# Performance work log

Hardware: AMD Instinct MI355X
Metric: run time of the kernel (lower is better)

Reference implementation:

```python
import jax, jax.numpy as jnp
import numpy as np

H = 8  # num_heads


def _ln(x, g, b):
    mu = x.mean(-1, keepdims=True)
    var = ((x - mu) ** 2).mean(-1, keepdims=True)
    return (x - mu) * jax.lax.rsqrt(var + 1e-5) * g + b


def setup_inputs() -> dict:
    key = jax.random.key(0)
    ks = jax.random.split(key, 24)
    B, N, V, E, D, R, L = 8, 512, 50000, 300, 256, 100, 4
    dh = D // H
    s = 0.02
    inp = {}
    inp['token_ids'] = jax.random.randint(ks[0], (B, N), 0, V, dtype=jnp.int32)
    inp['relations'] = jax.random.randint(ks[1], (B, N, N), 0, R, dtype=jnp.int32)
    m = jax.random.bernoulli(ks[2], 0.9, (B, N, N))
    eye = jnp.eye(N, dtype=bool)[None]
    inp['relations_mask'] = jnp.logical_or(m, eye)  # keep diagonal valid so every row attends somewhere
    inp['embed'] = jax.random.normal(ks[3], (V, E), jnp.float32) * s
    inp['W_in'] = jax.random.normal(ks[4], (E, D), jnp.float32) * s
    inp['b_in'] = jnp.zeros((D,), jnp.float32)
    inp['Wq'] = jax.random.normal(ks[5], (L, D, D), jnp.float32) * s
    inp['Wk'] = jax.random.normal(ks[6], (L, D, D), jnp.float32) * s
    inp['Wv'] = jax.random.normal(ks[7], (L, D, D), jnp.float32) * s
    inp['Wo'] = jax.random.normal(ks[8], (L, D, D), jnp.float32) * s
    inp['ln1_g'] = jnp.ones((L, D), jnp.float32)
    inp['ln1_b'] = jnp.zeros((L, D), jnp.float32)
    inp['ln2_g'] = jnp.ones((L, D), jnp.float32)
    inp['ln2_b'] = jnp.zeros((L, D), jnp.float32)
    inp['W1'] = jax.random.normal(ks[9], (L, D, 4 * D), jnp.float32) * s
    inp['b1'] = jnp.zeros((L, 4 * D), jnp.float32)
    inp['W2'] = jax.random.normal(ks[10], (L, 4 * D, D), jnp.float32) * s
    inp['b2'] = jnp.zeros((L, D), jnp.float32)
    inp['rel_k_emb'] = jax.random.normal(ks[11], (R, dh), jnp.float32) * s
    inp['rel_v_emb'] = jax.random.normal(ks[12], (R, dh), jnp.float32) * s
    inp['W_out'] = jax.random.normal(ks[13], (D, D), jnp.float32) * s
    inp['b_out'] = jnp.zeros((D,), jnp.float32)
    return inp


def reference(token_ids, relations, relations_mask, embed, W_in, b_in, Wq, Wk, Wv, Wo,
              ln1_g, ln1_b, ln2_g, ln2_b, W1, b1, W2, b2, rel_k_emb, rel_v_emb, W_out, b_out):
    # Input layer: embedding lookup + projection to gnn hidden size.
    x = embed[token_ids]                          # [B,N,E]
    x = jax.nn.relu(x @ W_in + b_in)              # [B,N,D]
    B, N, D = x.shape
    dh = D // H
    # Shared relation embeddings (share_layers=True, share_heads=True): gathered once.
    rk = rel_k_emb[relations]                     # [B,N,N,dh]
    rv = rel_v_emb[relations]                     # [B,N,N,dh]
    neg = jnp.asarray(-1e9, x.dtype)
    scale = jnp.asarray(1.0 / np.sqrt(dh), x.dtype)
    L = Wq.shape[0]
    for l in range(L):  # fixed small layer count
        q = (x @ Wq[l]).reshape(B, N, H, dh).transpose(0, 2, 1, 3)
        k = (x @ Wk[l]).reshape(B, N, H, dh).transpose(0, 2, 1, 3)
        v = (x @ Wv[l]).reshape(B, N, H, dh).transpose(0, 2, 1, 3)
        # Relation-aware scores: q.k + q.r_k (RAT-SQL)
        scores = (jnp.einsum('bhnd,bhmd->bhnm', q, k)
                  + jnp.einsum('bhnd,bnmd->bhnm', q, rk)) * scale
        scores = jnp.where(relations_mask[:, None], scores, neg)
        a = jax.nn.softmax(scores, axis=-1)       # [B,H,N,N]
        z = (jnp.einsum('bhnm,bhmd->bhnd', a, v)
             + jnp.einsum('bhnm,bnmd->bhnd', a, rv))
        z = z.transpose(0, 2, 1, 3).reshape(B, N, D) @ Wo[l]
        x = _ln(x + z, ln1_g[l], ln1_b[l])
        f = jax.nn.relu(x @ W1[l] + b1[l]) @ W2[l] + b2[l]
        x = _ln(x + f, ln2_g[l], ln2_b[l])
    # Output layer projection
    return x @ W_out + b_out
```

## Files before the change

### kernel.cpp

```cpp
#include <hip/hip_runtime.h>
#include <hip/hip_bf16.h>

#define NTOK 4096
#define NN   512

typedef __attribute__((ext_vector_type(8))) short bf16x8;
typedef __attribute__((ext_vector_type(4))) short bf16x4;
typedef __attribute__((ext_vector_type(4))) float f32x4;

__device__ __forceinline__ float bf16_to_f(unsigned short u) {
    unsigned int x = ((unsigned int)u) << 16;
    return __builtin_bit_cast(float, x);
}
__device__ __forceinline__ unsigned short f_to_bf16(float f) {
    unsigned int b = __builtin_bit_cast(unsigned int, f);
    return (unsigned short)((b + 0x7fff + ((b >> 16) & 1)) >> 16);
}
__device__ __forceinline__ bf16x8 pack8(float4 a, float4 b) {
    bf16x8 v;
    v[0]=(short)f_to_bf16(a.x); v[1]=(short)f_to_bf16(a.y);
    v[2]=(short)f_to_bf16(a.z); v[3]=(short)f_to_bf16(a.w);
    v[4]=(short)f_to_bf16(b.x); v[5]=(short)f_to_bf16(b.y);
    v[6]=(short)f_to_bf16(b.z); v[7]=(short)f_to_bf16(b.w);
    return v;
}

__global__ void detect_mask_kernel(const unsigned char* __restrict__ m, int* __restrict__ flag) {
    __shared__ int f;
    if (threadIdx.x == 0) f = 0;
    __syncthreads();
    int any = 0;
    for (int i = threadIdx.x; i < 4096; i += 256) {
        if ((i & 3) != 0 && m[i] != 0) any = 1;
    }
    if (any) atomicOr(&f, 1);
    __syncthreads();
    if (threadIdx.x == 0) *flag = f;
}

__global__ __launch_bounds__(256) void prep_rel16(
    const int* __restrict__ rel, const void* __restrict__ mask,
    const int* __restrict__ flag, short* __restrict__ rel16)
{
    const bool mbyte = (*flag != 0);
    const unsigned char* m8 = (const unsigned char*)mask;
    const int* m32 = (const int*)mask;
    const int i = (blockIdx.x * 256 + threadIdx.x) * 2;
    int2 rv = *(const int2*)(rel + i);
    int ok0, ok1;
    if (mbyte) { ok0 = m8[i]; ok1 = m8[i + 1]; }
    else       { ok0 = (m32[i] != 0); ok1 = (m32[i + 1] != 0); }
    short2 o;
    o.x = ok0 ? (short)rv.x : (short)-1;
    o.y = ok1 ? (short)rv.y : (short)-1;
    *(short2*)(rel16 + i) = o;
}

__global__ __launch_bounds__(256) void embed_proj_kernel(
    const int* __restrict__ tok, const float* __restrict__ embed,
    const float* __restrict__ W_in, const float* __restrict__ b_in,
    float* __restrict__ x)
{
    __shared__ float emb[8][304];
    __shared__ int tloc[8];
    const int t = threadIdx.x;
    const int r0 = blockIdx.x * 8;
    if (t < 8) tloc[t] = tok[r0 + t];
    __syncthreads();
    for (int i = t; i < 8 * 300; i += 256) {
        int r = i / 300, e = i - r * 300;
        emb[r][e] = embed[(size_t)tloc[r] * 300 + e];
    }
    __syncthreads();
    float acc[8] = {0.f,0.f,0.f,0.f,0.f,0.f,0.f,0.f};
    const int d = t;
    for (int e = 0; e < 300; ++e) {
        float w = W_in[e * 256 + d];
#pragma unroll
        for (int r = 0; r < 8; ++r) acc[r] += emb[r][e] * w;
    }
    const float bb = b_in[d];
#pragma unroll
    for (int r = 0; r < 8; ++r) {
        float o = acc[r] + bb;
        o = o > 0.f ? o : 0.f;
        x[(size_t)(r0 + r) * 256 + d] = o;
    }
}

__global__ __launch_bounds__(256) void gemm_mfma(
    const float* __restrict__ A,
    const float* __restrict__ W0, const float* __restrict__ W1p, const float* __restrict__ W2p,
    int ncPerW, const float* __restrict__ bias,
    float* __restrict__ C, int M, int K, int Nc, int relu)
{
    __shared__ unsigned short As[64][40];
    __shared__ unsigned short Bs[64][40];

    const int t = threadIdx.x;
    const int lane = t & 63, w = t >> 6;
    const int g = lane >> 4, li = lane & 15;
    const int r0 = blockIdx.y * 64, c0 = blockIdx.x * 64;

    const float* Wp = W0; int cW = c0;
    if (c0 >= 2 * ncPerW)      { Wp = W2p; cW = c0 - 2 * ncPerW; }
    else if (c0 >= ncPerW)     { Wp = W1p; cW = c0 - ncPerW; }

    f32x4 acc[4];
#pragma unroll
    for (int i = 0; i < 4; ++i) acc[i] = (f32x4){0.f, 0.f, 0.f, 0.f};

    const int arow = t >> 2, ad8 = (t & 3) * 8;
    const int bnn = t & 63, bk8 = (t >> 6) * 8;

    for (int k0 = 0; k0 < K; k0 += 32) {
        __syncthreads();
        {
            const float* ap = A + (size_t)(r0 + arow) * K + k0 + ad8;
            float4 a0 = *(const float4*)ap;
            float4 a1 = *(const float4*)(ap + 4);
            *(bf16x8*)&As[arow][ad8] = pack8(a0, a1);
        }
        {
            bf16x8 v;
#pragma unroll
            for (int j = 0; j < 8; ++j) {
                float xv = Wp[(size_t)(k0 + bk8 + j) * ncPerW + cW + bnn];
                v[j] = (short)f_to_bf16(xv);
            }
            *(bf16x8*)&Bs[bnn][bk8] = v;
        }
        __syncthreads();
        bf16x8 af = *(const bf16x8*)&As[16 * w + li][g * 8];
#pragma unroll
        for (int sub = 0; sub < 4; ++sub) {
            bf16x8 bfr = *(const bf16x8*)&Bs[16 * sub + li][g * 8];
            acc[sub] = __builtin_amdgcn_mfma_f32_16x16x32_bf16(af, bfr, acc[sub], 0, 0, 0);
        }
    }
#pragma unroll
    for (int sub = 0; sub < 4; ++sub) {
        int col = c0 + sub * 16 + li;
        float bv = bias ? bias[col] : 0.f;
#pragma unroll
        for (int r = 0; r < 4; ++r) {
            int row = r0 + 16 * w + g * 4 + r;
            float o = acc[sub][r] + bv;
            if (relu) o = fmaxf(o, 0.f);
            C[(size_t)row * Nc + col] = o;
        }
    }
}

__global__ __launch_bounds__(256) void attn_mfma(
    const float* __restrict__ qkv,
    const short* __restrict__ rel16,
    const float* __restrict__ relk_g,
    const float* __restrict__ relv_g,
    float* __restrict__ zout)
{
    const int b = blockIdx.z, h = blockIdx.y, n0 = blockIdx.x * 64;
    const int t = threadIdx.x;
    const int lane = t & 63, w = t >> 6;
    const int g = lane >> 4, li = lane & 15;

    __shared__ float wrel[64][100];
    __shared__ unsigned short qrk[64][100];
    __shared__ union {
        unsigned short relk_s[100][40];
        unsigned short relvT[32][136];
        struct {
            unsigned short k_t[32][40];
            unsigned short v_t[32][40];
            short rel_t[64][36];
            unsigned short p_s[4][16][40];
        } mn;
    } u;

    for (int i = t; i < 6400; i += 256) ((float*)wrel)[i] = 0.f;
    for (int i = t; i < 400; i += 256) {
        int rr = i >> 2, d8 = (i & 3) * 8;
        const float* sp = relk_g + rr * 32 + d8;
        *(bf16x8*)&u.relk_s[rr][d8] = pack8(*(const float4*)sp, *(const float4*)(sp + 4));
    }
    const float scale = 0.17677669529663687f;
    bf16x8 qf;
    {
        const float* qp = qkv + (size_t)(b * NN + n0 + 16 * w + li) * 768 + h * 32 + g * 8;
        float4 q0 = *(const float4*)qp, q1 = *(const float4*)(qp + 4);
        q0.x *= scale; q0.y *= scale; q0.z *= scale; q0.w *= scale;
        q1.x *= scale; q1.y *= scale; q1.z *= scale; q1.w *= scale;
        qf = pack8(q0, q1);
    }
    __syncthreads();

#pragma unroll
    for (int rc = 0; rc < 7; ++rc) {
        bf16x8 bb = *(const bf16x8*)&u.relk_s[rc * 16 + li][g * 8];
        f32x4 s = __builtin_amdgcn_mfma_f32_16x16x32_bf16(qf, bb, (f32x4){0.f,0.f,0.f,0.f}, 0, 0, 0);
        int col = rc * 16 + li;
        if (col < 100) {
#pragma unroll
            for (int r = 0; r < 4; ++r)
                qrk[16 * w + g * 4 + r][col] = f_to_bf16(s[r]);
        }
    }
    __syncthreads();

    float smacc[4] = {0.f, 0.f, 0.f, 0.f};
    f32x4 zf[2];
    zf[0] = (f32x4){0.f,0.f,0.f,0.f};
    zf[1] = (f32x4){0.f,0.f,0.f,0.f};
    const size_t relbase = ((size_t)b * NN + n0) * NN;

    for (int mt = 0; mt < 16; ++mt) {
        const int m0 = mt * 32;
        __syncthreads();
        {
            int row = t >> 3, d4 = (t & 7) * 4;
            const float* kp = qkv + (size_t)(b * NN + m0 + row) * 768 + 256 + h * 32 + d4;
            float4 kv4 = *(const float4*)kp;
            bf16x4 kv;
            kv[0]=(short)f_to_bf16(kv4.x); kv[1]=(short)f_to_bf16(kv4.y);
            kv[2]=(short)f_to_bf16(kv4.z); kv[3]=(short)f_to_bf16(kv4.w);
            *(bf16x4*)&u.mn.k_t[row][d4] = kv;
        }
        {
            int m = t & 31, dg = t >> 5;
            const float* vp = qkv + (size_t)(b * NN + m0 + m) * 768 + 512 + h * 32 + dg * 4;
            float4 vv = *(const float4*)vp;
            u.mn.v_t[dg * 4 + 0][m] = f_to_bf16(vv.x);
            u.mn.v_t[dg * 4 + 1][m] = f_to_bf16(vv.y);
            u.mn.v_t[dg * 4 + 2][m] = f_to_bf16(vv.z);
            u.mn.v_t[dg * 4 + 3][m] = f_to_bf16(vv.w);
        }
        {
#pragma unroll
            for (int ii = 0; ii < 2; ++ii) {
                int i = t * 2 + ii;
                int rr = i >> 3, m4 = (i & 7) * 4;
                int2 rv = *(const int2*)(rel16 + relbase + (size_t)rr * NN + m0 + m4);
                *(int2*)&u.mn.rel_t[rr][m4] = rv;
            }
        }
        __syncthreads();
#pragma unroll
        for (int c = 0; c < 2; ++c) {
            bf16x8 kf = *(const bf16x8*)&u.mn.k_t[c * 16 + li][g * 8];
            f32x4 s = __builtin_amdgcn_mfma_f32_16x16x32_bf16(qf, kf, (f32x4){0.f,0.f,0.f,0.f}, 0, 0, 0);
            const int mm = c * 16 + li;
#pragma unroll
            for (int r = 0; r < 4; ++r) {
                const int ql = 16 * w + g * 4 + r;
                const int rl = u.mn.rel_t[ql][mm];
                float p = 0.f;
                if (rl >= 0) {
                    float sc = s[r] + bf16_to_f(qrk[ql][rl]);
                    p = __expf(fminf(sc, 50.f));
                    atomicAdd(&wrel[ql][rl], p);
                }
                smacc[r] += p;
                u.mn.p_s[w][g * 4 + r][mm] = f_to_bf16(p);
            }
        }
        asm volatile("s_waitcnt lgkmcnt(0)" ::: "memory");
        __builtin_amdgcn_sched_barrier(0);
        bf16x8 pa = *(const bf16x8*)&u.mn.p_s[w][li][g * 8];
#pragma unroll
        for (int dc = 0; dc < 2; ++dc) {
            bf16x8 vb = *(const bf16x8*)&u.mn.v_t[dc * 16 + li][g * 8];
            zf[dc] = __builtin_amdgcn_mfma_f32_16x16x32_bf16(pa, vb, zf[dc], 0, 0, 0);
        }
    }
    __syncthreads();

    for (int i = t; i < 32 * 36; i += 256) {
        int d = i / 36, c = 100 + (i - (i / 36) * 36);
        u.relvT[d][c] = 0;
    }
    for (int i = t; i < 400; i += 256) {
        int rr = i >> 2, d8 = (i & 3) * 8;
        const float* sp = relv_g + rr * 32 + d8;
        float4 s0 = *(const float4*)sp, s1 = *(const float4*)(sp + 4);
        u.relvT[d8 + 0][rr] = f_to_bf16(s0.x);
        u.relvT[d8 + 1][rr] = f_to_bf16(s0.y);
        u.relvT[d8 + 2][rr] = f_to_bf16(s0.z);
        u.relvT[d8 + 3][rr] = f_to_bf16(s0.w);
        u.relvT[d8 + 4][rr] = f_to_bf16(s1.x);
        u.relvT[d8 + 5][rr] = f_to_bf16(s1.y);
        u.relvT[d8 + 6][rr] = f_to_bf16(s1.z);
        u.relvT[d8 + 7][rr] = f_to_bf16(s1.w);
    }
    __syncthreads();

#pragma unroll
    for (int kc = 0; kc < 4; ++kc) {
        const int kbase = kc * 32 + g * 8;
        const float* wp = &wrel[16 * w + li][0];
        bf16x8 af;
#pragma unroll
        for (int j = 0; j < 8; ++j) {
            int idx = kbase + j;
            float val = (idx < 100) ? wp[idx] : 0.f;
            af[j] = (short)f_to_bf16(val);
        }
#pragma unroll
        for (int dc = 0; dc < 2; ++dc) {
            bf16x8 vb = *(const bf16x8*)&u.relvT[dc * 16 + li][kbase];
            zf[dc] = __builtin_amdgcn_mfma_f32_16x16x32_bf16(af, vb, zf[dc], 0, 0, 0);
        }
    }

#pragma unroll
    for (int r = 0; r < 4; ++r) {
        smacc[r] += __shfl_xor(smacc[r], 1, 64);
        smacc[r] += __shfl_xor(smacc[r], 2, 64);
        smacc[r] += __shfl_xor(smacc[r], 4, 64);
        smacc[r] += __shfl_xor(smacc[r], 8, 64);
    }
#pragma unroll
    for (int r = 0; r < 4; ++r) {
        float inv = 1.f / smacc[r];
        size_t ob = ((size_t)(b * NN + n0 + 16 * w + g * 4 + r)) * 256 + h * 32;
#pragma unroll
        for (int dc = 0; dc < 2; ++dc)
            zout[ob + dc * 16 + li] = zf[dc][r] * inv;
    }
}

__global__ __launch_bounds__(256) void ln_kernel(
    const float* __restrict__ xin, const float* __restrict__ y,
    const float* __restrict__ g, const float* __restrict__ bsh,
    float* __restrict__ xout)
{
    const int t = threadIdx.x;
    const int w = t >> 6, lane = t & 63;
    const size_t row = (size_t)blockIdx.x * 4 + w;
    const float4 xv = *(const float4*)(xin + row * 256 + lane * 4);
    const float4 yv = *(const float4*)(y + row * 256 + lane * 4);
    float4 sv;
    sv.x = xv.x + yv.x; sv.y = xv.y + yv.y; sv.z = xv.z + yv.z; sv.w = xv.w + yv.w;
    float sum = sv.x + sv.y + sv.z + sv.w;
    float sq  = sv.x * sv.x + sv.y * sv.y + sv.z * sv.z + sv.w * sv.w;
#pragma unroll
    for (int off = 1; off < 64; off <<= 1) {
        sum += __shfl_xor(sum, off, 64);
        sq  += __shfl_xor(sq, off, 64);
    }
    const float mu = sum * (1.f / 256.f);
    const float var = sq * (1.f / 256.f) - mu * mu;
    const float rs = rsqrtf(var + 1e-5f);
    const float4 gv = *(const float4*)(g + lane * 4);
    const float4 bv = *(const float4*)(bsh + lane * 4);
    float4 o;
    o.x = (sv.x - mu) * rs * gv.x + bv.x;
    o.y = (sv.y - mu) * rs * gv.y + bv.y;
    o.z = (sv.z - mu) * rs * gv.z + bv.z;
    o.w = (sv.w - mu) * rs * gv.w + bv.w;
    *(float4*)(xout + row * 256 + lane * 4) = o;
}

extern "C" void kernel_launch(void* const* d_in, const int* in_sizes, int n_in,
                              void* d_out, int out_size, void* d_ws, size_t ws_size,
                              hipStream_t stream)
{
    (void)in_sizes; (void)n_in; (void)out_size;
    const int*   tok   = (const int*)d_in[0];
    const int*   rel   = (const int*)d_in[1];
    const void*  mask  = d_in[2];
    const float* embed = (const float*)d_in[3];
    const float* W_in  = (const float*)d_in[4];
    const float* b_in  = (const float*)d_in[5];
    const float* Wq    = (const float*)d_in[6];
    const float* Wk    = (const float*)d_in[7];
    const float* Wv    = (const float*)d_in[8];
    const float* Wo    = (const float*)d_in[9];
    const float* ln1g  = (const float*)d_in[10];
    const float* ln1b  = (const float*)d_in[11];
    const float* ln2g  = (const float*)d_in[12];
    const float* ln2b  = (const float*)d_in[13];
    const float* W1    = (const float*)d_in[14];
    const float* b1    = (const float*)d_in[15];
    const float* W2    = (const float*)d_in[16];
    const float* b2    = (const float*)d_in[17];
    const float* relk  = (const float*)d_in[18];
    const float* relv  = (const float*)d_in[19];
    const float* Wout  = (const float*)d_in[20];
    const float* bout  = (const float*)d_in[21];
    float* out = (float*)d_out;

    float* ws  = (float*)d_ws;
    float* x   = ws;
    float* z   = ws + (1u << 20);
    float* zo  = ws + 2u * (1u << 20);
    float* qkv = ws + 3u * (1u << 20);
    float* hb  = ws + 6u * (1u << 20);

    const bool roomy = ws_size >= ((size_t)48 << 20);
    short* rel16 = roomy ? (short*)(ws + 10u * (1u << 20)) : (short*)hb;
    int*   flag  = (int*)(ws + (roomy ? 11u : 10u) * (1u << 20));

    detect_mask_kernel<<<1, 256, 0, stream>>>((const unsigned char*)mask, flag);
    if (roomy)
        prep_rel16<<<4096, 256, 0, stream>>>(rel, mask, flag, rel16);
    embed_proj_kernel<<<512, 256, 0, stream>>>(tok, embed, W_in, b_in, x);

    for (int l = 0; l < 4; ++l) {
        const float* wq = Wq + (size_t)l * 65536;
        const float* wk = Wk + (size_t)l * 65536;
        const float* wv = Wv + (size_t)l * 65536;
        const float* wo = Wo + (size_t)l * 65536;
        const float* w1 = W1 + (size_t)l * 262144;
        const float* w2 = W2 + (size_t)l * 262144;

        if (!roomy)
            prep_rel16<<<4096, 256, 0, stream>>>(rel, mask, flag, rel16);

        gemm_mfma<<<dim3(12, 64), 256, 0, stream>>>(x, wq, wk, wv, 256, nullptr,
                                                    qkv, NTOK, 256, 768, 0);
        attn_mfma<<<dim3(8, 8, 8), 256, 0, stream>>>(qkv, rel16, relk, relv, z);
        gemm_mfma<<<dim3(4, 64), 256, 0, stream>>>(z, wo, wo, wo, 256, nullptr,
                                                   zo, NTOK, 256, 256, 0);
        ln_kernel<<<1024, 256, 0, stream>>>(x, zo, ln1g + l * 256, ln1b + l * 256, x);
        gemm_mfma<<<dim3(16, 64), 256, 0, stream>>>(x, w1, w1, w1, 1024, b1 + l * 1024,
                                                    hb, NTOK, 256, 1024, 1);
        gemm_mfma<<<dim3(4, 64), 256, 0, stream>>>(hb, w2, w2, w2, 256, b2 + l * 256,
                                                   zo, NTOK, 1024, 256, 0);
        ln_kernel<<<1024, 256, 0, stream>>>(x, zo, ln2g + l * 256, ln2b + l * 256, x);
    }
    gemm_mfma<<<dim3(4, 64), 256, 0, stream>>>(x, Wout, Wout, Wout, 256, bout,
                                               out, NTOK, 256, 256, 0);
}
```

Measured before the change: 755.2 us.

## Double-buffer GEMM and attention tiles with register prefetch, remap attention grid

The GEMM kernel now double-buffers its LDS A/B tiles and prefetches the next K-slice into registers while the current one is computed, which removes one barrier per iteration. The attention kernel does the same for its K and V tiles. It also reads relation ids straight from global memory into registers, one tile ahead, instead of staging them in LDS. The attention launch becomes a 1D grid with a swizzled block-to-(batch, head, row-tile) mapping, likely for better L2/XCD locality of the rel16 and K/V data. The cost is more registers and more LDS, which may lower occupancy.

```diff
diff --git a/kernel.cpp b/kernel.cpp
--- a/kernel.cpp
+++ b/kernel.cpp
@@ -94,8 +94,8 @@
     int ncPerW, const float* __restrict__ bias,
     float* __restrict__ C, int M, int K, int Nc, int relu)
 {
-    __shared__ unsigned short As[64][40];
-    __shared__ unsigned short Bs[64][40];
+    __shared__ unsigned short As[2][64][40];
+    __shared__ unsigned short Bs[2][64][40];
 
     const int t = threadIdx.x;
     const int lane = t & 63, w = t >> 6;
@@ -113,28 +113,38 @@
     const int arow = t >> 2, ad8 = (t & 3) * 8;
     const int bnn = t & 63, bk8 = (t >> 6) * 8;
 
-    for (int k0 = 0; k0 < K; k0 += 32) {
-        __syncthreads();
-        {
-            const float* ap = A + (size_t)(r0 + arow) * K + k0 + ad8;
-            float4 a0 = *(const float4*)ap;
-            float4 a1 = *(const float4*)(ap + 4);
-            *(bf16x8*)&As[arow][ad8] = pack8(a0, a1);
-        }
+    const float* ap0 = A + (size_t)(r0 + arow) * K + ad8;
+    float4 a0 = *(const float4*)ap0;
+    float4 a1 = *(const float4*)(ap0 + 4);
+    float wv[8];
+#pragma unroll
+    for (int j = 0; j < 8; ++j)
+        wv[j] = Wp[(size_t)(bk8 + j) * ncPerW + cW + bnn];
+
+    const int nk = K >> 5;
+    for (int ki = 0; ki < nk; ++ki) {
+        const int cur = ki & 1;
+        *(bf16x8*)&As[cur][arow][ad8] = pack8(a0, a1);
         {
             bf16x8 v;
 #pragma unroll
-            for (int j = 0; j < 8; ++j) {
-                float xv = Wp[(size_t)(k0 + bk8 + j) * ncPerW + cW + bnn];
-                v[j] = (short)f_to_bf16(xv);
-            }
-            *(bf16x8*)&Bs[bnn][bk8] = v;
+            for (int j = 0; j < 8; ++j) v[j] = (short)f_to_bf16(wv[j]);
+            *(bf16x8*)&Bs[cur][bnn][bk8] = v;
+        }
+        if (ki + 1 < nk) {
+            const int k0 = (ki + 1) * 32;
+            const float* ap = A + (size_t)(r0 + arow) * K + k0 + ad8;
+            a0 = *(const float4*)ap;
+            a1 = *(const float4*)(ap + 4);
+#pragma unroll
+            for (int j = 0; j < 8; ++j)
+                wv[j] = Wp[(size_t)(k0 + bk8 + j) * ncPerW + cW + bnn];
         }
         __syncthreads();
-        bf16x8 af = *(const bf16x8*)&As[16 * w + li][g * 8];
+        bf16x8 af = *(const bf16x8*)&As[cur][16 * w + li][g * 8];
 #pragma unroll
         for (int sub = 0; sub < 4; ++sub) {
-            bf16x8 bfr = *(const bf16x8*)&Bs[16 * sub + li][g * 8];
+            bf16x8 bfr = *(const bf16x8*)&Bs[cur][16 * sub + li][g * 8];
             acc[sub] = __builtin_amdgcn_mfma_f32_16x16x32_bf16(af, bfr, acc[sub], 0, 0, 0);
         }
     }
@@ -159,10 +169,17 @@
     const float* __restrict__ relv_g,
     float* __restrict__ zout)
 {
-    const int b = blockIdx.z, h = blockIdx.y, n0 = blockIdx.x * 64;
+    const int p = blockIdx.x;
+    const int cx = p & 7, kk = p >> 3;
+    const int bc = cx * 8 + (kk >> 3);
+    const int h  = kk & 7;
+    const int b  = bc >> 3;
+    const int n0 = (bc & 7) * 64;
+
     const int t = threadIdx.x;
     const int lane = t & 63, w = t >> 6;
     const int g = lane >> 4, li = lane & 15;
+    const int qrow = 16 * w + g * 4;
 
     __shared__ float wrel[64][100];
     __shared__ unsigned short qrk[64][100];
@@ -170,9 +187,8 @@
         unsigned short relk_s[100][40];
         unsigned short relvT[32][136];
         struct {
-            unsigned short k_t[32][40];
-            unsigned short v_t[32][40];
-            short rel_t[64][36];
+            unsigned short k_t[2][32][40];
+            unsigned short v_t[2][32][40];
             unsigned short p_s[4][16][40];
         } mn;
     } u;
@@ -202,75 +218,94 @@
         if (col < 100) {
 #pragma unroll
             for (int r = 0; r < 4; ++r)
-                qrk[16 * w + g * 4 + r][col] = f_to_bf16(s[r]);
-        }
-    }
-    __syncthreads();
+                qrk[qrow + r][col] = f_to_bf16(s[r]);
+        }
+    }
 
     float smacc[4] = {0.f, 0.f, 0.f, 0.f};
     f32x4 zf[2];
     zf[0] = (f32x4){0.f,0.f,0.f,0.f};
     zf[1] = (f32x4){0.f,0.f,0.f,0.f};
-    const size_t relbase = ((size_t)b * NN + n0) * NN;
+
+    const short* relrow[4];
+#pragma unroll
+    for (int r = 0; r < 4; ++r)
+        relrow[r] = rel16 + ((size_t)b * NN + n0 + qrow + r) * NN;
+
+    const int krow = t >> 3, kd4 = (t & 7) * 4;
+    const int vm = t & 31, vdg = t >> 5;
+    const size_t kbase0 = (size_t)(b * NN) * 768 + 256 + h * 32;
+    const size_t vbase0 = (size_t)(b * NN) * 768 + 512 + h * 32;
+
+    float4 kreg = *(const float4*)(qkv + kbase0 + (size_t)krow * 768 + kd4);
+    float4 vreg = *(const float4*)(qkv + vbase0 + (size_t)vm * 768 + vdg * 4);
+    short rr[8], rn[8];
+#pragma unroll
+    for (int idx = 0; idx < 8; ++idx)
+        rr[idx] = relrow[idx & 3][(idx >> 2) * 16 + li];
+
+    __syncthreads();
 
     for (int mt = 0; mt < 16; ++mt) {
-        const int m0 = mt * 32;
+        const int cur = mt & 1;
+        {
+            bf16x4 kv;
+            kv[0]=(short)f_to_bf16(kreg.x); kv[1]=(short)f_to_bf16(kreg.y);
+            kv[2]=(short)f_to_bf16(kreg.z); kv[3]=(short)f_to_bf16(kreg.w);
+            *(bf16x4*)&u.mn.k_t[cur][krow][kd4] = kv;
+        }
+        {
+            u.mn.v_t[cur][vdg * 4 + 0][vm] = f_to_bf16(vreg.x);
+            u.mn.v_t[cur][vdg * 4 + 1][vm] = f_to_bf16(vreg.y);
+            u.mn.v_t[cur][vdg * 4 + 2][vm] = f_to_bf16(vreg.z);
+            u.mn.v_t[cur][vdg * 4 + 3][vm] = f_to_bf16(vreg.w);
+        }
+        if (mt + 1 < 16) {
+            const int m0n = (mt + 1) * 32;
+            kreg = *(const float4*)(qkv + kbase0 + (size_t)(m0n + krow) * 768 + kd4);
+            vreg = *(const float4*)(qkv + vbase0 + (size_t)(m0n + vm) * 768 + vdg * 4);
+#pragma unroll
+            for (int idx = 0; idx < 8; ++idx)
+                rn[idx] = relrow[idx & 3][m0n + (idx >> 2) * 16 + li];
+        }
         __syncthreads();
-        {
-            int row = t >> 3, d4 = (t & 7) * 4;
-            const float* kp = qkv + (size_t)(b * NN + m0 + row) * 768 + 256 + h * 32 + d4;
-            float4 kv4 = *(const float4*)kp;
-            bf16x4 kv;
-            kv[0]=(short)f_to_bf16(kv4.x); kv[1]=(short)f_to_bf16(kv4.y);
-            kv[2]=(short)f_to_bf16(kv4.z); kv[3]=(short)f_to_bf16(kv4.w);
-            *(bf16x4*)&u.mn.k_t[row][d4] = kv;
-        }
-        {
-            int m = t & 31, dg = t >> 5;
-            const float* vp = qkv + (size_t)(b * NN + m0 + m) * 768 + 512 + h * 32 + dg * 4;
-            float4 vv = *(const float4*)vp;
-            u.mn.v_t[dg * 4 + 0][m] = f_to_bf16(vv.x);
-            u.mn.v_t[dg * 4 + 1][m] = f_to_bf16(vv.y);
-            u.mn.v_t[dg * 4 + 2][m] = f_to_bf16(vv.z);
-            u.mn.v_t[dg * 4 + 3][m] = f_to_bf16(vv.w);
-        }
-        {
-#pragma unroll
-            for (int ii = 0; ii < 2; ++ii) {
-                int i = t * 2 + ii;
-                int rr = i >> 3, m4 = (i & 7) * 4;
-                int2 rv = *(const int2*)(rel16 + relbase + (size_t)rr * NN + m0 + m4);
-                *(int2*)&u.mn.rel_t[rr][m4] = rv;
+
+        bf16x8 kf0 = *(const bf16x8*)&u.mn.k_t[cur][li][g * 8];
+        bf16x8 kf1 = *(const bf16x8*)&u.mn.k_t[cur][16 + li][g * 8];
+        f32x4 s0 = __builtin_amdgcn_mfma_f32_16x16x32_bf16(qf, kf0, (f32x4){0.f,0.f,0.f,0.f}, 0, 0, 0);
+        f32x4 s1 = __builtin_amdgcn_mfma_f32_16x16x32_bf16(qf, kf1, (f32x4){0.f,0.f,0.f,0.f}, 0, 0, 0);
+
+        float pr[8];
+#pragma unroll
+        for (int idx = 0; idx < 8; ++idx) {
+            const int r = idx & 3;
+            const int rl = rr[idx];
+            const int rla = rl < 0 ? 0 : rl;
+            const float qadd = bf16_to_f(qrk[qrow + r][rla]);
+            const float sv = ((idx >> 2) ? s1[r] : s0[r]) + qadd;
+            float pv = 0.f;
+            if (rl >= 0) {
+                pv = __expf(fminf(sv, 50.f));
+                atomicAdd(&wrel[qrow + r][rl], pv);
             }
-        }
-        __syncthreads();
-#pragma unroll
-        for (int c = 0; c < 2; ++c) {
-            bf16x8 kf = *(const bf16x8*)&u.mn.k_t[c * 16 + li][g * 8];
-            f32x4 s = __builtin_amdgcn_mfma_f32_16x16x32_bf16(qf, kf, (f32x4){0.f,0.f,0.f,0.f}, 0, 0, 0);
-            const int mm = c * 16 + li;
-#pragma unroll
-            for (int r = 0; r < 4; ++r) {
-                const int ql = 16 * w + g * 4 + r;
-                const int rl = u.mn.rel_t[ql][mm];
-                float p = 0.f;
-                if (rl >= 0) {
-                    float sc = s[r] + bf16_to_f(qrk[ql][rl]);
-                    p = __expf(fminf(sc, 50.f));
-                    atomicAdd(&wrel[ql][rl], p);
-                }
-                smacc[r] += p;
-                u.mn.p_s[w][g * 4 + r][mm] = f_to_bf16(p);
-            }
-        }
+            smacc[r] += pv;
+            pr[idx] = pv;
+        }
+#pragma unroll
+        for (int idx = 0; idx < 8; ++idx)
+            u.mn.p_s[w][g * 4 + (idx & 3)][(idx >> 2) * 16 + li] = f_to_bf16(pr[idx]);
+
         asm volatile("s_waitcnt lgkmcnt(0)" ::: "memory");
         __builtin_amdgcn_sched_barrier(0);
+
         bf16x8 pa = *(const bf16x8*)&u.mn.p_s[w][li][g * 8];
 #pragma unroll
         for (int dc = 0; dc < 2; ++dc) {
-            bf16x8 vb = *(const bf16x8*)&u.mn.v_t[dc * 16 + li][g * 8];
+            bf16x8 vb = *(const bf16x8*)&u.mn.v_t[cur][dc * 16 + li][g * 8];
             zf[dc] = __builtin_amdgcn_mfma_f32_16x16x32_bf16(pa, vb, zf[dc], 0, 0, 0);
         }
+#pragma unroll
+        for (int idx = 0; idx < 8; ++idx) rr[idx] = rn[idx];
     }
     __syncthreads();
 
@@ -279,17 +314,17 @@
         u.relvT[d][c] = 0;
     }
     for (int i = t; i < 400; i += 256) {
-        int rr = i >> 2, d8 = (i & 3) * 8;
-        const float* sp = relv_g + rr * 32 + d8;
+        int rr2 = i >> 2, d8 = (i & 3) * 8;
+        const float* sp = relv_g + rr2 * 32 + d8;
         float4 s0 = *(const float4*)sp, s1 = *(const float4*)(sp + 4);
-        u.relvT[d8 + 0][rr] = f_to_bf16(s0.x);
-        u.relvT[d8 + 1][rr] = f_to_bf16(s0.y);
-        u.relvT[d8 + 2][rr] = f_to_bf16(s0.z);
-        u.relvT[d8 + 3][rr] = f_to_bf16(s0.w);
-        u.relvT[d8 + 4][rr] = f_to_bf16(s1.x);
-        u.relvT[d8 + 5][rr] = f_to_bf16(s1.y);
-        u.relvT[d8 + 6][rr] = f_to_bf16(s1.z);
-        u.relvT[d8 + 7][rr] = f_to_bf16(s1.w);
+        u.relvT[d8 + 0][rr2] = f_to_bf16(s0.x);
+        u.relvT[d8 + 1][rr2] = f_to_bf16(s0.y);
+        u.relvT[d8 + 2][rr2] = f_to_bf16(s0.z);
+        u.relvT[d8 + 3][rr2] = f_to_bf16(s0.w);
+        u.relvT[d8 + 4][rr2] = f_to_bf16(s1.x);
+        u.relvT[d8 + 5][rr2] = f_to_bf16(s1.y);
+        u.relvT[d8 + 6][rr2] = f_to_bf16(s1.z);
+        u.relvT[d8 + 7][rr2] = f_to_bf16(s1.w);
     }
     __syncthreads();
 
@@ -321,7 +356,7 @@
 #pragma unroll
     for (int r = 0; r < 4; ++r) {
         float inv = 1.f / smacc[r];
-        size_t ob = ((size_t)(b * NN + n0 + 16 * w + g * 4 + r)) * 256 + h * 32;
+        size_t ob = ((size_t)(b * NN + n0 + qrow + r)) * 256 + h * 32;
 #pragma unroll
         for (int dc = 0; dc < 2; ++dc)
             zout[ob + dc * 16 + li] = zf[dc][r] * inv;
@@ -418,7 +453,7 @@
 
         gemm_mfma<<<dim3(12, 64), 256, 0, stream>>>(x, wq, wk, wv, 256, nullptr,
                                                     qkv, NTOK, 256, 768, 0);
-        attn_mfma<<<dim3(8, 8, 8), 256, 0, stream>>>(qkv, rel16, relk, relv, z);
+        attn_mfma<<<512, 256, 0, stream>>>(qkv, rel16, relk, relv, z);
         gemm_mfma<<<dim3(4, 64), 256, 0, stream>>>(z, wo, wo, wo, 256, nullptr,
                                                    zo, NTOK, 256, 256, 0);
         ln_kernel<<<1024, 256, 0, stream>>>(x, zo, ln1g + l * 256, ln1b + l * 256, x);
```

Result: faster. 638.0 us (-15.5%).
